# Kernel tuning notes

Hardware: AMD Instinct MI355X
Metric: run time of the kernel (lower is better)

Reference implementation:

```python
import jax, jax.numpy as jnp
import numpy as np

D = 4                      # corr_disp / max_displacement
K = 2 * D + 1              # window side -> K*K = 81 displacement channels
C = 256                    # in_channels


def shifted_patches(x, d):
    """x: [B,C,H,W] -> [B,C,K*K,H,W]; patch k=(dy*K+dx) is x shifted by
    (dy-d, dx-d) with zero padding (matches Correlation/NaiveAssemble2 indexing)."""
    B, Ch, H, W = x.shape
    xp = jnp.pad(x, ((0, 0), (0, 0), (d, d), (d, d)))
    k = 2 * d + 1
    sl = [xp[:, :, dy:dy + H, dx:dx + W] for dy in range(k) for dx in range(k)]
    return jnp.stack(sl, axis=2)


def conv2d(x, w, b, pad):
    y = jax.lax.conv_general_dilated(
        x, w, window_strides=(1, 1), padding=[(pad, pad), (pad, pad)],
        dimension_numbers=('NCHW', 'OIHW', 'NCHW'))
    return y + b[None, :, None, None]


def setup_inputs() -> dict:
    key = jax.random.key(0)
    ks = jax.random.split(key, 12)
    B, H, W = 2, 64, 64
    std = 0.01
    return {
        'feat':     jax.random.normal(ks[0], (B, C, H, W), jnp.float32),
        'feat_ref': jax.random.normal(ks[1], (B, C, H, W), jnp.float32),
        # ConcatUpdate conv stack: 2C->256 (1x1), 256->16 (3x3), 16->3 (3x3), 3->2 (3x3)
        'w1': jax.random.normal(ks[2], (256, 2 * C, 1, 1), jnp.float32) * std,
        'b1': jnp.zeros((256,), jnp.float32),
        'w2': jax.random.normal(ks[3], (16, 256, 3, 3), jnp.float32) * std,
        'b2': jnp.zeros((16,), jnp.float32),
        'w3': jax.random.normal(ks[4], (3, 16, 3, 3), jnp.float32) * std,
        'b3': jnp.zeros((3,), jnp.float32),
        'w4': jax.random.normal(ks[5], (2, 3, 3, 3), jnp.float32) * std,
        'b4': jnp.array([1.0, 0.0], jnp.float32),  # init_weights: bias[0]=1, bias[1]=0
    }


def reference(feat, feat_ref, w1, b1, w2, b2, w3, b3, w4, b4):
    # Correlation (cost volume over (2D+1)^2 displacements, kernel_size=1)
    patches = shifted_patches(feat_ref, D)                    # [B,C,K2,H,W]
    aff = jnp.einsum('bchw,bckhw->bkhw', feat, patches)       # [B,K2,H,W]
    # sum-normalize over displacement channels (use_softmax_norm=False)
    aff = aff / (jnp.sum(aff, axis=1, keepdims=True) + 1e-7)
    # NaiveAssemble2: windowed weighted gather of feat_ref
    aligned = jnp.einsum('bkhw,bckhw->bchw', aff, patches)    # [B,C,H,W]
    # ConcatUpdate
    cat = jnp.concatenate([feat, aligned], axis=1)            # [B,2C,H,W]
    h = conv2d(cat, w1, b1, 0)
    h = conv2d(h, w2, b2, 1)
    h = conv2d(h, w3, b3, 1)
    logits = conv2d(h, w4, b4, 1)                             # [B,2,H,W]
    score = jax.nn.softmax(logits, axis=1)
    return score[:, 0:1] * feat + score[:, 1:2] * aligned
```

## Files before the change

### kernel.cpp

```cpp
#include <hip/hip_runtime.h>
#include <hip/hip_bf16.h>
#include <math.h>

#define BATCH 2
#define CCH   256
#define HH    64
#define WW    64
#define PIX   (HH*WW)
#define K2    81
#define BP_N  (BATCH*PIX)

__global__ void k_transpose2(const float* __restrict__ feat,
                             const float* __restrict__ feat_ref,
                             float* __restrict__ featT,
                             float* __restrict__ refT) {
    __shared__ float tile[32][33];
    int z  = blockIdx.z;
    int b  = z & 1;
    const float* in  = (z >> 1) ? feat_ref : feat;
    float*       out = (z >> 1) ? refT     : featT;
    int p0 = blockIdx.x * 32;
    int c0 = blockIdx.y * 32;
    int tx = threadIdx.x;
    int ty = threadIdx.y;
    const float* ib = in  + (size_t)b * CCH * PIX;
    float*       ob = out + (size_t)b * CCH * PIX;
    #pragma unroll
    for (int i = 0; i < 4; i++) {
        int c = c0 + ty + i * 8;
        int p = p0 + tx;
        tile[ty + i * 8][tx] = ib[(size_t)c * PIX + p];
    }
    __syncthreads();
    #pragma unroll
    for (int i = 0; i < 4; i++) {
        int p = p0 + ty + i * 8;
        int c = c0 + tx;
        ob[(size_t)p * CCH + c] = tile[tx][ty + i * 8];
    }
}

__global__ void k_wprep(const float* __restrict__ w1, float* __restrict__ w1t,
                        const float* __restrict__ w2, float* __restrict__ w2t) {
    __shared__ float tile[32][33];
    int blk = blockIdx.x;
    int tid = threadIdx.x;
    if (blk < 128) {
        int c0 = (blk & 15) * 32;
        int o0 = (blk >> 4) * 32;
        int tx = tid & 31;
        int ty = tid >> 5;
        #pragma unroll
        for (int i = 0; i < 4; i++)
            tile[ty + i * 8][tx] = w1[(size_t)(o0 + ty + i * 8) * 512 + c0 + tx];
        __syncthreads();
        #pragma unroll
        for (int i = 0; i < 4; i++)
            w1t[(size_t)(c0 + ty + i * 8) * 256 + o0 + tx] = tile[tx][ty + i * 8];
    } else {
        int i = (blk - 128) * 256 + tid;
        if (i < 16 * 256 * 9) {
            int o  = i / 2304;
            int r  = i % 2304;
            int c  = r / 9;
            int kk = r % 9;
            int cg = c >> 2, ci = c & 3;
            w2t[(((kk * 64 + cg) * 16 + o) << 2) + ci] = w2[i];
        }
    }
}

__global__ void k_corr_assemble(const float* __restrict__ featT,
                                const float* __restrict__ refT,
                                float* __restrict__ alignedT) {
    int blk = blockIdx.x;
    int pr  = ((blk & 7) << 9) | (blk >> 3);
    int bp  = pr << 1;
    int b  = bp >> 12;
    int p  = bp & 4095;
    int h  = p >> 6, w = p & 63;
    int tid = threadIdx.x;

    __shared__ float s_aff0[K2];
    __shared__ float s_aff1[K2];
    __shared__ __align__(8) int2 s_u[96];
    __shared__ int   s_hi_a[32];
    __shared__ int   s_hi_b[32];
    __shared__ int   s_cnt0, s_cnt1;
    __shared__ float s_den0, s_den1;
    __shared__ __align__(16) float s_c0[96];
    __shared__ __align__(16) float s_c1[96];
    __shared__ __align__(16) int   s_po[96];

    int hw = tid >> 5;
    int j  = tid & 31;

    const float* fb = featT + ((size_t)bp << 8) + j;
    float f0[8], f1[8];
    #pragma unroll
    for (int t = 0; t < 8; t++) { f0[t] = fb[32 * t]; f1[t] = fb[256 + 32 * t]; }

    if (tid < K2) { s_aff0[tid] = 0.f; s_aff1[tid] = 0.f; }

    if (tid < 128) {
        int u  = tid;
        int uy = u / 10, ux = u - uy * 10;
        int y  = h + uy - 4, x = w + ux - 4;
        bool valid = (u < 90) && ((unsigned)y < 64u) && ((unsigned)x < 64u);
        int poff = ((y << 6) | x) << 10;
        int meta = (ux << 8) | (uy * 9 + ux);
        unsigned long long m = __ballot(valid);
        int lane   = tid & 63;
        int prefix = __popcll(m & ((1ULL << lane) - 1ULL));
        if (tid < 64) {
            if (valid) s_u[prefix] = make_int2(poff, meta);
            if (tid == 0) s_cnt0 = (int)__popcll(m);
        } else {
            if (valid) { s_hi_a[prefix] = poff; s_hi_b[prefix] = meta; }
            if (tid == 64) s_cnt1 = (int)__popcll(m);
        }
    }
    __syncthreads();
    int n0 = s_cnt0, n1 = s_cnt1;
    int nu = n0 + n1;
    if (tid < n1) s_u[n0 + tid] = make_int2(s_hi_a[tid], s_hi_b[tid]);
    __syncthreads();

    const float* rb  = refT + ((size_t)b << 20);
    const char*  rbj = (const char*)rb + 4 * j;

    for (int ii = 2 * hw; ii < nu; ii += 16) {
        int2 U0 = s_u[ii];
        bool has1 = (ii + 1) < nu;
        int2 U1 = has1 ? s_u[ii + 1] : U0;
        const char* rp0 = rbj + U0.x;
        const char* rp1 = rbj + U1.x;
        float r0[8], r1[8];
        #pragma unroll
        for (int t = 0; t < 8; t++) {
            r0[t] = *(const float*)(rp0 + 128 * t);
            r1[t] = *(const float*)(rp1 + 128 * t);
        }
        float pa0 = 0.f, pb0 = 0.f, pa1 = 0.f, pb1 = 0.f;
        #pragma unroll
        for (int t = 0; t < 8; t++) {
            pa0 = fmaf(f0[t], r0[t], pa0);
            pb0 = fmaf(f1[t], r0[t], pb0);
            pa1 = fmaf(f0[t], r1[t], pa1);
            pb1 = fmaf(f1[t], r1[t], pb1);
        }
        pa0 = __fadd_rn(pa0, __shfl_xor(pa0, 8));
        pb0 = __fadd_rn(pb0, __shfl_xor(pb0, 8));
        pa1 = __fadd_rn(pa1, __shfl_xor(pa1, 8));
        pb1 = __fadd_rn(pb1, __shfl_xor(pb1, 8));
        pa0 = __fadd_rn(pa0, __shfl_xor(pa0, 16));
        pb0 = __fadd_rn(pb0, __shfl_xor(pb0, 16));
        pa1 = __fadd_rn(pa1, __shfl_xor(pa1, 16));
        pb1 = __fadd_rn(pb1, __shfl_xor(pb1, 16));
        pa0 = __fadd_rn(pa0, __shfl_xor(pa0, 4));
        pb0 = __fadd_rn(pb0, __shfl_xor(pb0, 4));
        pa1 = __fadd_rn(pa1, __shfl_xor(pa1, 4));
        pb1 = __fadd_rn(pb1, __shfl_xor(pb1, 4));
        pa0 = __fadd_rn(pa0, __shfl_xor(pa0, 2));
        pb0 = __fadd_rn(pb0, __shfl_xor(pb0, 2));
        pa1 = __fadd_rn(pa1, __shfl_xor(pa1, 2));
        pb1 = __fadd_rn(pb1, __shfl_xor(pb1, 2));
        pa0 = __fadd_rn(pa0, __shfl_xor(pa0, 1));
        pb0 = __fadd_rn(pb0, __shfl_xor(pb0, 1));
        pa1 = __fadd_rn(pa1, __shfl_xor(pa1, 1));
        pb1 = __fadd_rn(pb1, __shfl_xor(pb1, 1));
        if (j == 0) {
            int k0 = U0.y & 255, ux0 = U0.y >> 8;
            if (ux0 < 9) s_aff0[k0] = pa0;
            if (ux0 > 0) s_aff1[k0 - 1] = pb0;
            if (has1) {
                int k1 = U1.y & 255, ux1 = U1.y >> 8;
                if (ux1 < 9) s_aff0[k1] = pa1;
                if (ux1 > 0) s_aff1[k1 - 1] = pb1;
            }
        }
    }
    __syncthreads();

    if (tid < 2) {
        const float* sa = tid ? s_aff1 : s_aff0;
        float s = 0.f;
        for (int k = 0; k < K2; k++) s = __fadd_rn(s, sa[k]);
        float d = __fadd_rn(s, 1e-7f);
        if (tid) s_den1 = d; else s_den0 = d;
    }
    __syncthreads();

    if (tid < nu) {
        int2 uu = s_u[tid];
        int k0 = uu.y & 255, ux = uu.y >> 8;
        s_po[tid] = uu.x;
        s_c0[tid] = (ux < 9) ? __fdiv_rn(s_aff0[k0], s_den0) : 0.f;
        s_c1[tid] = (ux > 0) ? __fdiv_rn(s_aff1[k0 - 1], s_den1) : 0.f;
    }
    __syncthreads();

    const char* rbc = (const char*)rb + ((size_t)tid << 2);
    float a0 = 0.f, a1 = 0.f;
    int i = 0;
    for (; i + 8 <= nu; i += 8) {
        float4 cA0 = *(const float4*)&s_c0[i];
        float4 cA1 = *(const float4*)&s_c0[i + 4];
        float4 cB0 = *(const float4*)&s_c1[i];
        float4 cB1 = *(const float4*)&s_c1[i + 4];
        int4   poA = *(const int4*)&s_po[i];
        int4   poB = *(const int4*)&s_po[i + 4];
        float v0 = *(const float*)(rbc + poA.x);
        float v1 = *(const float*)(rbc + poA.y);
        float v2 = *(const float*)(rbc + poA.z);
        float v3 = *(const float*)(rbc + poA.w);
        float v4 = *(const float*)(rbc + poB.x);
        float v5 = *(const float*)(rbc + poB.y);
        float v6 = *(const float*)(rbc + poB.z);
        float v7 = *(const float*)(rbc + poB.w);
        a0 = fmaf(cA0.x, v0, a0);  a1 = fmaf(cB0.x, v0, a1);
        a0 = fmaf(cA0.y, v1, a0);  a1 = fmaf(cB0.y, v1, a1);
        a0 = fmaf(cA0.z, v2, a0);  a1 = fmaf(cB0.z, v2, a1);
        a0 = fmaf(cA0.w, v3, a0);  a1 = fmaf(cB0.w, v3, a1);
        a0 = fmaf(cA1.x, v4, a0);  a1 = fmaf(cB1.x, v4, a1);
        a0 = fmaf(cA1.y, v5, a0);  a1 = fmaf(cB1.y, v5, a1);
        a0 = fmaf(cA1.z, v6, a0);  a1 = fmaf(cB1.z, v6, a1);
        a0 = fmaf(cA1.w, v7, a0);  a1 = fmaf(cB1.w, v7, a1);
    }
    if (i + 4 <= nu) {
        float4 cA = *(const float4*)&s_c0[i];
        float4 cB = *(const float4*)&s_c1[i];
        int4   po = *(const int4*)&s_po[i];
        float v0 = *(const float*)(rbc + po.x);
        float v1 = *(const float*)(rbc + po.y);
        float v2 = *(const float*)(rbc + po.z);
        float v3 = *(const float*)(rbc + po.w);
        a0 = fmaf(cA.x, v0, a0);  a1 = fmaf(cB.x, v0, a1);
        a0 = fmaf(cA.y, v1, a0);  a1 = fmaf(cB.y, v1, a1);
        a0 = fmaf(cA.z, v2, a0);  a1 = fmaf(cB.z, v2, a1);
        a0 = fmaf(cA.w, v3, a0);  a1 = fmaf(cB.w, v3, a1);
        i += 4;
    }
    for (; i < nu; i++) {
        float v = *(const float*)(rbc + s_po[i]);
        a0 = fmaf(s_c0[i], v, a0);
        a1 = fmaf(s_c1[i], v, a1);
    }
    alignedT[((size_t)bp << 8) + tid]       = a0;
    alignedT[((size_t)(bp + 1) << 8) + tid] = a1;
}

__global__ void k_conv1(const float* __restrict__ featT,
                        const float* __restrict__ alignedT,
                        const float* __restrict__ w1t,
                        const float* __restrict__ b1,
                        float* __restrict__ h1) {
    __shared__ float s_a[32][68];
    __shared__ float s_b[32][68];
    int m0  = blockIdx.x * 64;
    int n0  = blockIdx.y * 64;
    int tid = threadIdx.x;
    int tx  = tid & 15;
    int ty  = tid >> 4;

    float acc[4][4] = {{0.f}};

    for (int kc = 0; kc < 16; kc++) {
        int c0 = kc * 32;
        const float* asrc;
        int coff;
        if (c0 < 256) { asrc = featT;    coff = c0; }
        else          { asrc = alignedT; coff = c0 - 256; }

        #pragma unroll
        for (int i = tid; i < 512; i += 256) {
            int cq = i & 7, px = i >> 3;
            float4 v = *(const float4*)(asrc + ((size_t)(m0 + px) << 8) + coff + (cq << 2));
            s_a[cq * 4 + 0][px] = v.x;
            s_a[cq * 4 + 1][px] = v.y;
            s_a[cq * 4 + 2][px] = v.z;
            s_a[cq * 4 + 3][px] = v.w;
        }
        #pragma unroll
        for (int i = tid; i < 512; i += 256) {
            int oq = i & 15, cc = i >> 4;
            float4 v = *(const float4*)(w1t + (size_t)(c0 + cc) * 256 + n0 + (oq << 2));
            *(float4*)&s_b[cc][oq << 2] = v;
        }
        __syncthreads();

        #pragma unroll 8
        for (int k = 0; k < 32; k++) {
            float4 av = *(const float4*)&s_a[k][ty << 2];
            float4 bv = *(const float4*)&s_b[k][tx << 2];
            acc[0][0] = fmaf(av.x, bv.x, acc[0][0]);
            acc[0][1] = fmaf(av.x, bv.y, acc[0][1]);
            acc[0][2] = fmaf(av.x, bv.z, acc[0][2]);
            acc[0][3] = fmaf(av.x, bv.w, acc[0][3]);
            acc[1][0] = fmaf(av.y, bv.x, acc[1][0]);
            acc[1][1] = fmaf(av.y, bv.y, acc[1][1]);
            acc[1][2] = fmaf(av.y, bv.z, acc[1][2]);
            acc[1][3] = fmaf(av.y, bv.w, acc[1][3]);
            acc[2][0] = fmaf(av.z, bv.x, acc[2][0]);
            acc[2][1] = fmaf(av.z, bv.y, acc[2][1]);
            acc[2][2] = fmaf(av.z, bv.z, acc[2][2]);
            acc[2][3] = fmaf(av.z, bv.w, acc[2][3]);
            acc[3][0] = fmaf(av.w, bv.x, acc[3][0]);
            acc[3][1] = fmaf(av.w, bv.y, acc[3][1]);
            acc[3][2] = fmaf(av.w, bv.z, acc[3][2]);
            acc[3][3] = fmaf(av.w, bv.w, acc[3][3]);
        }
        __syncthreads();
    }

    float4 bias = *(const float4*)(b1 + n0 + tx * 4);
    #pragma unroll
    for (int i = 0; i < 4; i++) {
        int px = m0 + ty * 4 + i;
        float4 v;
        v.x = acc[i][0] + bias.x;
        v.y = acc[i][1] + bias.y;
        v.z = acc[i][2] + bias.z;
        v.w = acc[i][3] + bias.w;
        *(float4*)(h1 + ((size_t)px << 8) + n0 + tx * 4) = v;
    }
}

__global__ void k_conv2(const float* __restrict__ h1,
                        const float* __restrict__ w2t,
                        const float* __restrict__ b2,
                        float* __restrict__ h2) {
    __shared__ float s_in[3][18][68];
    int blk = blockIdx.x;
    int b   = blk >> 8;
    int r   = blk & 255;
    int y   = r >> 2;
    int w0  = (r & 3) * 16;
    int tid = threadIdx.x;
    int o   = tid & 15;
    int ps  = (tid >> 4) & 7;

    const float* hb = h1 + ((size_t)b << 20);

    float4 a0 = {0.f, 0.f, 0.f, 0.f};
    float4 a1 = {0.f, 0.f, 0.f, 0.f};

    for (int chunk = 0; chunk < 4; chunk++) {
        int c0 = chunk << 6;
        for (int i = tid; i < 3 * 18 * 16; i += 256) {
            int c4 = i & 15;
            int pi = (i >> 4) % 18;
            int ri = (i >> 4) / 18;
            int yy = y + ri - 1;
            int xx = w0 + pi - 1;
            float4 v = {0.f, 0.f, 0.f, 0.f};
            if ((unsigned)yy < 64u && (unsigned)xx < 64u)
                v = *(const float4*)(hb + ((size_t)((yy << 6) | xx) << 8) + c0 + (c4 << 2));
            *(float4*)&s_in[ri][pi][c4 << 2] = v;
        }
        __syncthreads();

        #pragma unroll
        for (int kk = 0; kk < 9; kk++) {
            int ky = kk / 3, kx = kk - ky * 3;
            const float* wp = w2t + (((size_t)(kk * 64 + (c0 >> 2)) * 16 + o) << 2);
            #pragma unroll 8
            for (int c4 = 0; c4 < 16; c4++) {
                float4 wv = *(const float4*)(wp + (c4 << 6));
                float4 i0 = *(const float4*)&s_in[ky][ps + kx][c4 << 2];
                float4 i1 = *(const float4*)&s_in[ky][ps + 8 + kx][c4 << 2];
                a0.x = fmaf(wv.x, i0.x, a0.x);
                a0.y = fmaf(wv.y, i0.y, a0.y);
                a0.z = fmaf(wv.z, i0.z, a0.z);
                a0.w = fmaf(wv.w, i0.w, a0.w);
                a1.x = fmaf(wv.x, i1.x, a1.x);
                a1.y = fmaf(wv.y, i1.y, a1.y);
                a1.z = fmaf(wv.z, i1.z, a1.z);
                a1.w = fmaf(wv.w, i1.w, a1.w);
            }
        }
        __syncthreads();
    }

    size_t bp0 = ((size_t)b << 12) + (y << 6) + w0;
    h2[(bp0 + ps) * 16 + o]     = ((a0.x + a0.y) + (a0.z + a0.w)) + b2[o];
    h2[(bp0 + ps + 8) * 16 + o] = ((a1.x + a1.y) + (a1.z + a1.w)) + b2[o];
}

__global__ void k_conv3(const float* __restrict__ h2,
                        const float* __restrict__ w3,
                        const float* __restrict__ b3,
                        float* __restrict__ h3) {
    int bp = blockIdx.x * 256 + threadIdx.x;
    if (bp >= BP_N) return;
    int b = bp >> 12;
    int p = bp & 4095;
    int h = p >> 6, w = p & 63;
    const float* hb = h2 + ((size_t)b << 16);

    float a0 = 0.f, a1 = 0.f, a2 = 0.f;
    #pragma unroll
    for (int kk = 0; kk < 9; kk++) {
        int ky = kk / 3, kx = kk - ky * 3;
        int y = h + ky - 1, x = w + kx - 1;
        if ((unsigned)y >= 64u || (unsigned)x >= 64u) continue;
        const float* ip = hb + (size_t)((y << 6) | x) * 16;
        #pragma unroll
        for (int c = 0; c < 16; c++) {
            float v = ip[c];
            int wi = c * 9 + kk;
            a0 = fmaf(w3[wi],       v, a0);
            a1 = fmaf(w3[144 + wi], v, a1);
            a2 = fmaf(w3[288 + wi], v, a2);
        }
    }
    h3[(size_t)bp * 3 + 0] = a0 + b3[0];
    h3[(size_t)bp * 3 + 1] = a1 + b3[1];
    h3[(size_t)bp * 3 + 2] = a2 + b3[2];
}

__global__ void k_score(const float* __restrict__ h3,
                        const float* __restrict__ w4,
                        const float* __restrict__ b4,
                        float2* __restrict__ score) {
    int bp = blockIdx.x * 256 + threadIdx.x;
    if (bp >= BP_N) return;
    int b = bp >> 12;
    int p = bp & 4095;
    int h = p >> 6, w = p & 63;
    const float* hb = h3 + (size_t)b * PIX * 3;

    float l0 = 0.f, l1 = 0.f;
    #pragma unroll
    for (int kk = 0; kk < 9; kk++) {
        int ky = kk / 3, kx = kk - ky * 3;
        int y = h + ky - 1, x = w + kx - 1;
        if ((unsigned)y >= 64u || (unsigned)x >= 64u) continue;
        const float* ip = hb + (size_t)((y << 6) | x) * 3;
        #pragma unroll
        for (int c = 0; c < 3; c++) {
            float v = ip[c];
            int wi = c * 9 + kk;
            l0 = fmaf(w4[wi],      v, l0);
            l1 = fmaf(w4[27 + wi], v, l1);
        }
    }
    l0 += b4[0];
    l1 += b4[1];

    float m  = fmaxf(l0, l1);
    float e0 = expf(l0 - m);
    float e1 = expf(l1 - m);
    float s  = e0 + e1;
    score[bp] = make_float2(e0 / s, e1 / s);
}

__global__ void k_blend(const float* __restrict__ feat,
                        const float* __restrict__ alignedT,
                        const float2* __restrict__ score,
                        float* __restrict__ out) {
    __shared__ float tile[32][33];
    int b  = blockIdx.z;
    int p0 = blockIdx.x * 32;
    int c0 = blockIdx.y * 32;
    int tx = threadIdx.x;
    int ty = threadIdx.y;

    const float* at = alignedT + ((size_t)b << 20);
    #pragma unroll
    for (int i = 0; i < 4; i++) {
        int p = p0 + ty + i * 8;
        tile[ty + i * 8][tx] = at[((size_t)p << 8) + c0 + tx];
    }
    __syncthreads();

    int p = p0 + tx;
    float2 s = score[(b << 12) + p];
    #pragma unroll
    for (int i = 0; i < 4; i++) {
        int c = c0 + ty + i * 8;
        size_t idx = (((size_t)(b * 256 + c)) << 12) + p;
        out[idx] = __fadd_rn(__fmul_rn(s.x, feat[idx]),
                             __fmul_rn(s.y, tile[tx][ty + i * 8]));
    }
}

extern "C" void kernel_launch(void* const* d_in, const int* in_sizes, int n_in,
                              void* d_out, int out_size, void* d_ws, size_t ws_size,
                              hipStream_t stream) {
    const float* feat     = (const float*)d_in[0];
    const float* feat_ref = (const float*)d_in[1];
    const float* w1 = (const float*)d_in[2];
    const float* b1 = (const float*)d_in[3];
    const float* w2 = (const float*)d_in[4];
    const float* b2 = (const float*)d_in[5];
    const float* w3 = (const float*)d_in[6];
    const float* b3 = (const float*)d_in[7];
    const float* w4 = (const float*)d_in[8];
    const float* b4 = (const float*)d_in[9];
    float* out = (float*)d_out;

    const size_t NCP = (size_t)BATCH * CCH * PIX;
    char* wsb = (char*)d_ws;
    float*  featT    = (float*)wsb;   wsb += NCP * 4;
    float*  refT     = (float*)wsb;   wsb += NCP * 4;
    float*  alignedT = (float*)wsb;   wsb += NCP * 4;
    float*  h1       = (float*)wsb;   wsb += NCP * 4;
    float*  h2       = (float*)wsb;   wsb += (size_t)BP_N * 16 * 4;
    float*  h3       = (float*)wsb;   wsb += (size_t)BP_N * 3 * 4;
    float2* sc       = (float2*)wsb;  wsb += (size_t)BP_N * 8;
    float*  w2t      = (float*)wsb;   wsb += (size_t)16 * 256 * 9 * 4;
    float*  w1t      = (float*)wsb;   wsb += (size_t)512 * 256 * 4;

    dim3 tb(32, 8, 1);
    k_transpose2<<<dim3(PIX / 32, CCH / 32, 4), tb, 0, stream>>>(feat, feat_ref, featT, refT);
    k_wprep<<<272, 256, 0, stream>>>(w1, w1t, w2, w2t);

    k_corr_assemble<<<BP_N / 2, 256, 0, stream>>>(featT, refT, alignedT);
    k_conv1<<<dim3(BP_N / 64, 256 / 64, 1), 256, 0, stream>>>(featT, alignedT, w1t, b1, h1);
    k_conv2<<<BP_N / 16, 256, 0, stream>>>(h1, w2t, b2, h2);
    k_conv3<<<BP_N / 256, 256, 0, stream>>>(h2, w3, b3, h3);
    k_score<<<BP_N / 256, 256, 0, stream>>>(h3, w4, b4, sc);
    k_blend<<<dim3(PIX / 32, CCH / 32, BATCH), tb, 0, stream>>>(feat, alignedT, sc, out);
}
```

Before: 221.8 us.

## Software-pipeline correlation gather loads and double-buffer conv1 shared tiles

The correlation loop now prefetches the next iteration's feat_ref values into registers before running the current iteration's shuffle reduction. This is meant to hide global load latency behind the reductions. The 1x1 conv GEMM kernel now double-buffers its shared-memory tiles and issues the global loads for the next K-chunk before computing on the current one, which removes one barrier per iteration. Both changes raise register use and conv1 doubles its shared memory, which may lower occupancy.

```diff
diff --git a/kernel.cpp b/kernel.cpp
--- a/kernel.cpp
+++ b/kernel.cpp
@@ -129,18 +129,24 @@
     const float* rb  = refT + ((size_t)b << 20);
     const char*  rbj = (const char*)rb + 4 * j;
 
-    for (int ii = 2 * hw; ii < nu; ii += 16) {
-        int2 U0 = s_u[ii];
-        bool has1 = (ii + 1) < nu;
-        int2 U1 = has1 ? s_u[ii + 1] : U0;
+    int ii = 2 * hw;
+    bool act = ii < nu;
+    int2 U0 = make_int2(0, 0), U1 = make_int2(0, 0);
+    bool has1 = false;
+    float r0[8], r1[8];
+    if (act) {
+        U0 = s_u[ii];
+        has1 = (ii + 1) < nu;
+        U1 = has1 ? s_u[ii + 1] : U0;
         const char* rp0 = rbj + U0.x;
         const char* rp1 = rbj + U1.x;
-        float r0[8], r1[8];
         #pragma unroll
         for (int t = 0; t < 8; t++) {
             r0[t] = *(const float*)(rp0 + 128 * t);
             r1[t] = *(const float*)(rp1 + 128 * t);
         }
+    }
+    while (act) {
         float pa0 = 0.f, pb0 = 0.f, pa1 = 0.f, pb1 = 0.f;
         #pragma unroll
         for (int t = 0; t < 8; t++) {
@@ -149,6 +155,24 @@
             pa1 = fmaf(f0[t], r1[t], pa1);
             pb1 = fmaf(f1[t], r1[t], pb1);
         }
+        int  m0c = U0.y, m1c = U1.y;
+        bool h1c = has1;
+
+        ii += 16;
+        bool nact = ii < nu;
+        if (nact) {
+            U0 = s_u[ii];
+            has1 = (ii + 1) < nu;
+            U1 = has1 ? s_u[ii + 1] : U0;
+            const char* rp0 = rbj + U0.x;
+            const char* rp1 = rbj + U1.x;
+            #pragma unroll
+            for (int t = 0; t < 8; t++) {
+                r0[t] = *(const float*)(rp0 + 128 * t);
+                r1[t] = *(const float*)(rp1 + 128 * t);
+            }
+        }
+
         pa0 = __fadd_rn(pa0, __shfl_xor(pa0, 8));
         pb0 = __fadd_rn(pb0, __shfl_xor(pb0, 8));
         pa1 = __fadd_rn(pa1, __shfl_xor(pa1, 8));
@@ -170,15 +194,16 @@
         pa1 = __fadd_rn(pa1, __shfl_xor(pa1, 1));
         pb1 = __fadd_rn(pb1, __shfl_xor(pb1, 1));
         if (j == 0) {
-            int k0 = U0.y & 255, ux0 = U0.y >> 8;
+            int k0 = m0c & 255, ux0 = m0c >> 8;
             if (ux0 < 9) s_aff0[k0] = pa0;
             if (ux0 > 0) s_aff1[k0 - 1] = pb0;
-            if (has1) {
-                int k1 = U1.y & 255, ux1 = U1.y >> 8;
+            if (h1c) {
+                int k1 = m1c & 255, ux1 = m1c >> 8;
                 if (ux1 < 9) s_aff0[k1] = pa1;
                 if (ux1 > 0) s_aff1[k1 - 1] = pb1;
             }
         }
+        act = nact;
     }
     __syncthreads();
 
@@ -255,44 +280,56 @@
                         const float* __restrict__ w1t,
                         const float* __restrict__ b1,
                         float* __restrict__ h1) {
-    __shared__ float s_a[32][68];
-    __shared__ float s_b[32][68];
+    __shared__ float s_a[2][32][68];
+    __shared__ float s_b[2][32][68];
     int m0  = blockIdx.x * 64;
     int n0  = blockIdx.y * 64;
     int tid = threadIdx.x;
     int tx  = tid & 15;
     int ty  = tid >> 4;
+    int cq  = tid & 7;
+    int pxa = tid >> 3;
+    int oq  = tid & 15;
+    int cc  = tid >> 4;
 
     float acc[4][4] = {{0.f}};
+    float4 ra0, ra1, rb0, rb1;
+
+#define C1_LOAD(kc_) do {                                                     \
+        int c0_ = (kc_) * 32;                                                 \
+        const float* asrc_ = (c0_ < 256) ? featT : alignedT;                  \
+        int coff_ = (c0_ < 256) ? c0_ : c0_ - 256;                            \
+        ra0 = *(const float4*)(asrc_ + ((size_t)(m0 + pxa) << 8) + coff_ + (cq << 2));      \
+        ra1 = *(const float4*)(asrc_ + ((size_t)(m0 + 32 + pxa) << 8) + coff_ + (cq << 2)); \
+        rb0 = *(const float4*)(w1t + (size_t)(c0_ + cc) * 256 + n0 + (oq << 2));            \
+        rb1 = *(const float4*)(w1t + (size_t)(c0_ + 16 + cc) * 256 + n0 + (oq << 2));       \
+    } while (0)
+
+#define C1_WRITE(bf_) do {                                                    \
+        s_a[bf_][cq * 4 + 0][pxa] = ra0.x;                                    \
+        s_a[bf_][cq * 4 + 1][pxa] = ra0.y;                                    \
+        s_a[bf_][cq * 4 + 2][pxa] = ra0.z;                                    \
+        s_a[bf_][cq * 4 + 3][pxa] = ra0.w;                                    \
+        s_a[bf_][cq * 4 + 0][32 + pxa] = ra1.x;                               \
+        s_a[bf_][cq * 4 + 1][32 + pxa] = ra1.y;                               \
+        s_a[bf_][cq * 4 + 2][32 + pxa] = ra1.z;                               \
+        s_a[bf_][cq * 4 + 3][32 + pxa] = ra1.w;                               \
+        *(float4*)&s_b[bf_][cc][oq << 2] = rb0;                               \
+        *(float4*)&s_b[bf_][16 + cc][oq << 2] = rb1;                          \
+    } while (0)
+
+    C1_LOAD(0);
+    C1_WRITE(0);
+    __syncthreads();
 
     for (int kc = 0; kc < 16; kc++) {
-        int c0 = kc * 32;
-        const float* asrc;
-        int coff;
-        if (c0 < 256) { asrc = featT;    coff = c0; }
-        else          { asrc = alignedT; coff = c0 - 256; }
-
-        #pragma unroll
-        for (int i = tid; i < 512; i += 256) {
-            int cq = i & 7, px = i >> 3;
-            float4 v = *(const float4*)(asrc + ((size_t)(m0 + px) << 8) + coff + (cq << 2));
-            s_a[cq * 4 + 0][px] = v.x;
-            s_a[cq * 4 + 1][px] = v.y;
-            s_a[cq * 4 + 2][px] = v.z;
-            s_a[cq * 4 + 3][px] = v.w;
-        }
-        #pragma unroll
-        for (int i = tid; i < 512; i += 256) {
-            int oq = i & 15, cc = i >> 4;
-            float4 v = *(const float4*)(w1t + (size_t)(c0 + cc) * 256 + n0 + (oq << 2));
-            *(float4*)&s_b[cc][oq << 2] = v;
-        }
-        __syncthreads();
+        int cur = kc & 1;
+        if (kc < 15) C1_LOAD(kc + 1);
 
         #pragma unroll 8
         for (int k = 0; k < 32; k++) {
-            float4 av = *(const float4*)&s_a[k][ty << 2];
-            float4 bv = *(const float4*)&s_b[k][tx << 2];
+            float4 av = *(const float4*)&s_a[cur][k][ty << 2];
+            float4 bv = *(const float4*)&s_b[cur][k][tx << 2];
             acc[0][0] = fmaf(av.x, bv.x, acc[0][0]);
             acc[0][1] = fmaf(av.x, bv.y, acc[0][1]);
             acc[0][2] = fmaf(av.x, bv.z, acc[0][2]);
@@ -310,6 +347,8 @@
             acc[3][2] = fmaf(av.w, bv.z, acc[3][2]);
             acc[3][3] = fmaf(av.w, bv.w, acc[3][3]);
         }
+
+        if (kc < 15) C1_WRITE(cur ^ 1);
         __syncthreads();
     }
 
```

Result: faster. 216.5 us (-2.4%).
